# Kernel optimization log

Hardware: AMD Instinct MI355X
Metric: run time of the kernel (lower is better)

## Reference

```python
import jax, jax.numpy as jnp
import numpy as np

ORDER = 3  # truncation level; num_components = ORDER*(ORDER+1)//2 = 6 (independent weights)


def setup_inputs() -> dict:
    key = jax.random.key(0)
    k1, k2, k3 = jax.random.split(key, 3)
    B, T, D, F = 64, 4096, 128, 64
    C = ORDER * (ORDER + 1) // 2
    sequences = jax.random.normal(k1, (B, T, D), dtype=jnp.float32)
    # ls2t_uniform-style init: scaled uniform per component
    kernel = jax.random.normal(k2, (C, D, F), dtype=jnp.float32) / np.sqrt(D)
    bias = jax.random.normal(k3, (C, F), dtype=jnp.float32) * 0.01
    return {"sequences": sequences, "kernel": kernel, "bias": bias}


def _exclusive_cumsum(x, axis):
    # exclusive cumsum = inclusive cumsum minus self (avoids concat/pad allocs)
    return jnp.cumsum(x, axis=axis) - x


def reference(sequences, kernel, bias):
    # sequences: [B, T, D]; kernel: [C, D, F]; bias: [C, F]
    # M[c] = sequences @ kernel[c] + bias[c]  -> [C, B, T, F]
    M = jnp.einsum('btd,cdf->cbtf', sequences, kernel) + bias[:, None, None, :]
    # Level 1: plain sum over time of first component
    Y = [jnp.sum(M[0], axis=1)]  # [B, F]
    k = 1
    for m in range(1, ORDER):
        R = M[k]
        k += 1
        for _ in range(m):
            # iterated-sum recursion: strictly-lower-triangular (exclusive) cumsum over time
            R = M[k] * _exclusive_cumsum(R, axis=1)
            k += 1
        Y.append(jnp.sum(R, axis=1))
    return jnp.stack(Y, axis=-1)  # [B, F, ORDER]
```

## Files before the change

### kernel.cpp

```cpp
#include <hip/hip_runtime.h>
#include <hip/hip_bf16.h>


#define B_ 64
#define T_ 4096
#define D_ 128
#define F_ 64
#define TGROUPS 8
#define TB 512
#define CHT 16
#define NITER (TB / CHT)
#define TPB 512
#define RING 4

typedef __attribute__((ext_vector_type(8))) short short8v;
typedef __attribute__((ext_vector_type(4))) float f32x4;
typedef __attribute__((ext_vector_type(4))) unsigned short ushort4v;

__device__ __forceinline__ unsigned short bfb(float x) {
    __hip_bfloat16 h = __float2bfloat16(x);
    unsigned short u;
    __builtin_memcpy(&u, &h, 2);
    return u;
}

#define BAR() asm volatile("s_waitcnt lgkmcnt(0)\n\ts_barrier" ::: "memory")

__global__ __launch_bounds__(TPB, 2)
void ls2t_kernel(const float* __restrict__ seq,
                 const float* __restrict__ kern,
                 const float* __restrict__ bias,
                 float* __restrict__ ws)
{
    __shared__ unsigned short slds[RING][CHT * D_];

    const int tid  = threadIdx.x;
    const int tg   = blockIdx.x;
    const int b    = blockIdx.y;
    const int lane = tid & 63;
    const int w    = tid >> 6;
    const int cg   = w >> 2;
    const int wv   = w & 3;
    const int fr   = lane & 15;
    const int lg   = lane >> 4;
    const int f    = wv * 16 + fr;

    short8v bfrag[3][4];
    float bc[3];
    #pragma unroll
    for (int cc = 0; cc < 3; ++cc) {
        const int c = cg * 3 + cc;
        bc[cc] = bias[c * F_ + f];
        #pragma unroll
        for (int ks = 0; ks < 4; ++ks) {
            const float* kp = kern + ((size_t)c * D_ + ks * 32 + lg * 8) * F_ + f;
            short8v bf;
            #pragma unroll
            for (int j = 0; j < 8; ++j) bf[j] = (short)bfb(kp[(size_t)j * F_]);
            bfrag[cc][ks] = bf;
        }
    }

    const float* sbase = seq + ((size_t)b * T_ + (size_t)tg * TB) * D_;

    const int srow = tid >> 5;
    const int c4   = tid & 31;
    const int skey = srow & 7;
    const float* g0 = sbase + ((size_t)((srow >> 2) * 128 + (srow & 3))) * D_ + c4 * 4;
    const int woff = srow * D_ + 8 * ((c4 >> 1) ^ skey) + 4 * (c4 & 1);

    #define LD(i) (*reinterpret_cast<const float4*>(g0 + (size_t)(i) * 4 * D_))

    auto wst = [&](int bufi, const float4& v) {
        ushort4v u;
        u[0] = bfb(v.x); u[1] = bfb(v.y); u[2] = bfb(v.z); u[3] = bfb(v.w);
        *reinterpret_cast<ushort4v*>(&slds[bufi][woff]) = u;
    };

    float a0 = 0.f, s1 = 0.f, s2 = 0.f, q2 = 0.f;
    float su = 0.f, sv = 0.f, sw = 0.f, qvu = 0.f, qwv = 0.f, qwvu = 0.f;

    auto compute = [&](int bufi) {
        f32x4 acc[3];
        #pragma unroll
        for (int cc = 0; cc < 3; ++cc)
            acc[cc] = (f32x4){bc[cc], bc[cc], bc[cc], bc[cc]};

        #pragma unroll
        for (int ks = 0; ks < 4; ++ks) {
            const int m0i = ks * 4 + lg;
            short8v a = *reinterpret_cast<const short8v*>(
                &slds[bufi][fr * D_ + 8 * (m0i ^ (fr & 7))]);
            #pragma unroll
            for (int cc = 0; cc < 3; ++cc)
                acc[cc] = __builtin_amdgcn_mfma_f32_16x16x32_bf16(
                    a, bfrag[cc][ks], acc[cc], 0, 0, 0);
        }

        if (cg == 0) {
            #pragma unroll
            for (int r = 0; r < 4; ++r) {
                float m0 = acc[0][r], m1 = acc[1][r], m2 = acc[2][r];
                a0 += m0;
                q2  = fmaf(m2, s1, q2);
                s2 += m2;
                s1 += m1;
            }
        } else {
            #pragma unroll
            for (int r = 0; r < 4; ++r) {
                float m3 = acc[0][r], m4 = acc[1][r], m5 = acc[2][r];
                qwvu = fmaf(m5, qvu, qwvu);
                qwv  = fmaf(m5, sv, qwv);
                sw  += m5;
                qvu  = fmaf(m4, su, qvu);
                sv  += m4;
                su  += m3;
            }
        }
    };

    float4 v0 = LD(0), v1 = LD(1), v2 = LD(2), v3 = LD(3);
    wst(0, v0);
    BAR();

    #pragma unroll 1
    for (int g = 0; g < 7; ++g) {
        const int i = g * 4;
        v0 = LD(i + 4);
        wst(1, v1);
        BAR();
        compute(0);
        v1 = LD(i + 5);
        wst(2, v2);
        BAR();
        compute(1);
        v2 = LD(i + 6);
        wst(3, v3);
        BAR();
        compute(2);
        v3 = LD(i + 7);
        wst(0, v0);
        BAR();
        compute(3);
    }
    wst(1, v1); BAR(); compute(0);
    wst(2, v2); BAR(); compute(1);
    wst(3, v3); BAR(); compute(2);
    compute(3);

    if (cg == 0) {
        #pragma unroll
        for (int m = 16; m <= 32; m <<= 1) {
            float oa0 = __shfl_xor(a0, m), os1 = __shfl_xor(s1, m);
            float os2 = __shfl_xor(s2, m), oq2 = __shfl_xor(q2, m);
            bool up = (lane & m) != 0;
            float Aa0 = up ? oa0 : a0, As1 = up ? os1 : s1;
            float As2 = up ? os2 : s2, Aq2 = up ? oq2 : q2;
            float Ba0 = up ? a0 : oa0, Bs1 = up ? s1 : os1;
            float Bs2 = up ? s2 : os2, Bq2 = up ? q2 : oq2;
            a0 = Aa0 + Ba0;
            q2 = Aq2 + Bq2 + As1 * Bs2;
            s1 = As1 + Bs1;
            s2 = As2 + Bs2;
        }
        if (lg == 0) {
            float* wp = ws + (((size_t)b * TGROUPS + tg) * F_ + f) * 10;
            wp[0] = a0; wp[1] = s1; wp[2] = s2; wp[3] = q2;
        }
    } else {
        #pragma unroll
        for (int m = 16; m <= 32; m <<= 1) {
            float osu = __shfl_xor(su, m),  osv = __shfl_xor(sv, m);
            float osw = __shfl_xor(sw, m),  oqvu = __shfl_xor(qvu, m);
            float oqwv = __shfl_xor(qwv, m), oqwvu = __shfl_xor(qwvu, m);
            bool up = (lane & m) != 0;
            float Asu = up ? osu : su,   Asv = up ? osv : sv;
            float Asw = up ? osw : sw,   Aqvu = up ? oqvu : qvu;
            float Aqwv = up ? oqwv : qwv, Aqwvu = up ? oqwvu : qwvu;
            float Bsu = up ? su : osu,   Bsv = up ? sv : osv;
            float Bsw = up ? sw : osw,   Bqvu = up ? qvu : oqvu;
            float Bqwv = up ? qwv : oqwv, Bqwvu = up ? qwvu : oqwvu;
            qwvu = Aqwvu + Bqwvu + Aqvu * Bsw + Asu * Bqwv;
            qwv  = Aqwv + Bqwv + Asv * Bsw;
            qvu  = Aqvu + Bqvu + Asu * Bsv;
            su = Asu + Bsu;
            sv = Asv + Bsv;
            sw = Asw + Bsw;
        }
        if (lg == 0) {
            float* wp = ws + (((size_t)b * TGROUPS + tg) * F_ + f) * 10;
            wp[4] = su; wp[5] = sv; wp[6] = sw;
            wp[7] = qvu; wp[8] = qwv; wp[9] = qwvu;
        }
    }
    #undef LD
}

struct St { float a0, s1, s2, q2, su, sv, sw, qvu, qwv, qwvu; };

__device__ __forceinline__ St mergeSt(const St& A, const St& B) {
    St r;
    r.a0   = A.a0 + B.a0;
    r.q2   = A.q2 + B.q2 + A.s1 * B.s2;
    r.s1   = A.s1 + B.s1;
    r.s2   = A.s2 + B.s2;
    r.qwvu = A.qwvu + B.qwvu + A.qvu * B.sw + A.su * B.qwv;
    r.qwv  = A.qwv + B.qwv + A.sv * B.sw;
    r.qvu  = A.qvu + B.qvu + A.su * B.sv;
    r.su   = A.su + B.su;
    r.sv   = A.sv + B.sv;
    r.sw   = A.sw + B.sw;
    return r;
}

__global__ __launch_bounds__(64)
void ls2t_fold_kernel(const float* __restrict__ ws, float* __restrict__ out)
{
    const int b = blockIdx.x;
    const int f = threadIdx.x;
    St A = {0, 0, 0, 0, 0, 0, 0, 0, 0, 0};
    #pragma unroll
    for (int g = 0; g < TGROUPS; ++g) {
        const float* rp = ws + (((size_t)b * TGROUPS + g) * F_ + f) * 10;
        St r = {rp[0], rp[1], rp[2], rp[3], rp[4],
                rp[5], rp[6], rp[7], rp[8], rp[9]};
        A = mergeSt(A, r);
    }
    float* op = out + ((size_t)b * F_ + f) * 3;
    op[0] = A.a0;
    op[1] = A.q2;
    op[2] = A.qwvu;
}

extern "C" void kernel_launch(void* const* d_in, const int* in_sizes, int n_in,
                              void* d_out, int out_size, void* d_ws, size_t ws_size,
                              hipStream_t stream) {
    const float* seq  = (const float*)d_in[0];
    const float* kern = (const float*)d_in[1];
    const float* bias = (const float*)d_in[2];
    float* out = (float*)d_out;
    float* ws  = (float*)d_ws;

    dim3 g1(TGROUPS, B_);
    ls2t_kernel<<<g1, TPB, 0, stream>>>(seq, kern, bias, ws);
    ls2t_fold_kernel<<<B_, F_, 0, stream>>>(ws, out);
}
```

Baseline: 45.43 us.

## Double time groups, widen LDS chunks, and use truncating bf16 pack

Halves the time block per workgroup to 256 (16 time groups, 1024 workgroups) and doubles the LDS chunk to 32 rows, with two float4 loads per thread and two 16-row MFMA sub-tiles per chunk. Replaces round-to-nearest bf16 conversion with a byte-permute that truncates the high halves. The aim is more grid parallelism, fewer barriers per row, and cheaper conversion. The cost is a larger LDS ring, more partial states for the fold kernel to merge, and slightly changed rounding.

```diff
diff --git a/kernel.cpp b/kernel.cpp
--- a/kernel.cpp
+++ b/kernel.cpp
@@ -6,16 +6,15 @@
 #define T_ 4096
 #define D_ 128
 #define F_ 64
-#define TGROUPS 8
-#define TB 512
-#define CHT 16
+#define TB 256
+#define TGROUPS (T_ / TB)
+#define CHT 32
 #define NITER (TB / CHT)
 #define TPB 512
 #define RING 4
 
 typedef __attribute__((ext_vector_type(8))) short short8v;
 typedef __attribute__((ext_vector_type(4))) float f32x4;
-typedef __attribute__((ext_vector_type(4))) unsigned short ushort4v;
 
 __device__ __forceinline__ unsigned short bfb(float x) {
     __hip_bfloat16 h = __float2bfloat16(x);
@@ -63,83 +62,110 @@
 
     const float* sbase = seq + ((size_t)b * T_ + (size_t)tg * TB) * D_;
 
-    const int srow = tid >> 5;
-    const int c4   = tid & 31;
-    const int skey = srow & 7;
-    const float* g0 = sbase + ((size_t)((srow >> 2) * 128 + (srow & 3))) * D_ + c4 * 4;
-    const int woff = srow * D_ + 8 * ((c4 >> 1) ^ skey) + 4 * (c4 & 1);
-
-    #define LD(i) (*reinterpret_cast<const float4*>(g0 + (size_t)(i) * 4 * D_))
-
-    auto wst = [&](int bufi, const float4& v) {
-        ushort4v u;
-        u[0] = bfb(v.x); u[1] = bfb(v.y); u[2] = bfb(v.z); u[3] = bfb(v.w);
-        *reinterpret_cast<ushort4v*>(&slds[bufi][woff]) = u;
+    const float* gp[2];
+    int woff[2];
+    #pragma unroll
+    for (int k = 0; k < 2; ++k) {
+        const int u  = k * TPB + tid;
+        const int v  = u >> 5, c4 = u & 31;
+        const int bv = ((v >> 2) & 3) * 64 + ((v >> 4) << 2) + (v & 3);
+        gp[k]   = sbase + (size_t)bv * D_ + c4 * 4;
+        woff[k] = v * D_ + 8 * ((c4 >> 1) ^ (v & 7)) + 4 * (c4 & 1);
+    }
+
+    struct VSet { float4 a, b; };
+    auto issue = [&](int i, VSet& vs) {
+        vs.a = *reinterpret_cast<const float4*>(gp[0] + (size_t)i * 8 * D_);
+        vs.b = *reinterpret_cast<const float4*>(gp[1] + (size_t)i * 8 * D_);
+    };
+    auto wst = [&](int bufi, const VSet& vs) {
+        unsigned short* L = &slds[bufi][0];
+        {
+            unsigned p0 = __builtin_amdgcn_perm(__float_as_uint(vs.a.y),
+                                                __float_as_uint(vs.a.x), 0x07060302u);
+            unsigned p1 = __builtin_amdgcn_perm(__float_as_uint(vs.a.w),
+                                                __float_as_uint(vs.a.z), 0x07060302u);
+            uint2 pv; pv.x = p0; pv.y = p1;
+            *reinterpret_cast<uint2*>(&L[woff[0]]) = pv;
+        }
+        {
+            unsigned p0 = __builtin_amdgcn_perm(__float_as_uint(vs.b.y),
+                                                __float_as_uint(vs.b.x), 0x07060302u);
+            unsigned p1 = __builtin_amdgcn_perm(__float_as_uint(vs.b.w),
+                                                __float_as_uint(vs.b.z), 0x07060302u);
+            uint2 pv; pv.x = p0; pv.y = p1;
+            *reinterpret_cast<uint2*>(&L[woff[1]]) = pv;
+        }
     };
 
     float a0 = 0.f, s1 = 0.f, s2 = 0.f, q2 = 0.f;
     float su = 0.f, sv = 0.f, sw = 0.f, qvu = 0.f, qwv = 0.f, qwvu = 0.f;
 
     auto compute = [&](int bufi) {
-        f32x4 acc[3];
-        #pragma unroll
-        for (int cc = 0; cc < 3; ++cc)
-            acc[cc] = (f32x4){bc[cc], bc[cc], bc[cc], bc[cc]};
-
-        #pragma unroll
-        for (int ks = 0; ks < 4; ++ks) {
-            const int m0i = ks * 4 + lg;
-            short8v a = *reinterpret_cast<const short8v*>(
-                &slds[bufi][fr * D_ + 8 * (m0i ^ (fr & 7))]);
+        #pragma unroll
+        for (int s = 0; s < 2; ++s) {
+            f32x4 acc[3];
             #pragma unroll
             for (int cc = 0; cc < 3; ++cc)
-                acc[cc] = __builtin_amdgcn_mfma_f32_16x16x32_bf16(
-                    a, bfrag[cc][ks], acc[cc], 0, 0, 0);
-        }
-
-        if (cg == 0) {
+                acc[cc] = (f32x4){bc[cc], bc[cc], bc[cc], bc[cc]};
+
             #pragma unroll
-            for (int r = 0; r < 4; ++r) {
-                float m0 = acc[0][r], m1 = acc[1][r], m2 = acc[2][r];
-                a0 += m0;
-                q2  = fmaf(m2, s1, q2);
-                s2 += m2;
-                s1 += m1;
+            for (int ks = 0; ks < 4; ++ks) {
+                short8v a = *reinterpret_cast<const short8v*>(
+                    &slds[bufi][(s * 16 + fr) * D_ + 8 * ((ks * 4 + lg) ^ (fr & 7))]);
+                #pragma unroll
+                for (int cc = 0; cc < 3; ++cc)
+                    acc[cc] = __builtin_amdgcn_mfma_f32_16x16x32_bf16(
+                        a, bfrag[cc][ks], acc[cc], 0, 0, 0);
             }
-        } else {
-            #pragma unroll
-            for (int r = 0; r < 4; ++r) {
-                float m3 = acc[0][r], m4 = acc[1][r], m5 = acc[2][r];
-                qwvu = fmaf(m5, qvu, qwvu);
-                qwv  = fmaf(m5, sv, qwv);
-                sw  += m5;
-                qvu  = fmaf(m4, su, qvu);
-                sv  += m4;
-                su  += m3;
+
+            if (cg == 0) {
+                #pragma unroll
+                for (int r = 0; r < 4; ++r) {
+                    float m0 = acc[0][r], m1 = acc[1][r], m2 = acc[2][r];
+                    a0 += m0;
+                    q2  = fmaf(m2, s1, q2);
+                    s2 += m2;
+                    s1 += m1;
+                }
+            } else {
+                #pragma unroll
+                for (int r = 0; r < 4; ++r) {
+                    float m3 = acc[0][r], m4 = acc[1][r], m5 = acc[2][r];
+                    qwvu = fmaf(m5, qvu, qwvu);
+                    qwv  = fmaf(m5, sv, qwv);
+                    sw  += m5;
+                    qvu  = fmaf(m4, su, qvu);
+                    sv  += m4;
+                    su  += m3;
+                }
             }
         }
     };
 
-    float4 v0 = LD(0), v1 = LD(1), v2 = LD(2), v3 = LD(3);
+    VSet v0, v1, v2, v3;
+    issue(0, v0); issue(1, v1); issue(2, v2); issue(3, v3);
     wst(0, v0);
     BAR();
 
     #pragma unroll 1
-    for (int g = 0; g < 7; ++g) {
-        const int i = g * 4;
-        v0 = LD(i + 4);
+    for (int g = 0; g + 4 < NITER; g += 4) {
+        issue(g + 4, v0);
         wst(1, v1);
         BAR();
         compute(0);
-        v1 = LD(i + 5);
+
+        issue(g + 5, v1);
         wst(2, v2);
         BAR();
         compute(1);
-        v2 = LD(i + 6);
+
+        issue(g + 6, v2);
         wst(3, v3);
         BAR();
         compute(2);
-        v3 = LD(i + 7);
+
+        issue(g + 7, v3);
         wst(0, v0);
         BAR();
         compute(3);
@@ -194,7 +220,6 @@
             wp[7] = qvu; wp[8] = qwv; wp[9] = qwvu;
         }
     }
-    #undef LD
 }
 
 struct St { float a0, s1, s2, q2, su, sv, sw, qvu, qwv, qwvu; };
```

Result: slower. 64.55 us (+42.1%).

## Deepen LDS ring to eight slots and process two chunks per barrier

Applied to the files above, without the earlier changes.

The LDS ring buffer grows from 4 to 8 chunk slots. Each pipeline step now loads, converts and stores two 16-row chunks and runs two MFMA compute passes between barriers, which halves the number of barriers and keeps more global loads in flight. The cost is twice the shared memory per block (32 KB) and more live float4 registers, which could lower occupancy or add register pressure.

```diff
diff --git a/kernel.cpp b/kernel.cpp
--- a/kernel.cpp
+++ b/kernel.cpp
@@ -6,12 +6,12 @@
 #define T_ 4096
 #define D_ 128
 #define F_ 64
-#define TGROUPS 8
 #define TB 512
+#define TGROUPS (T_ / TB)
 #define CHT 16
 #define NITER (TB / CHT)
 #define TPB 512
-#define RING 4
+#define RING 8
 
 typedef __attribute__((ext_vector_type(8))) short short8v;
 typedef __attribute__((ext_vector_type(4))) float f32x4;
@@ -65,9 +65,8 @@
 
     const int srow = tid >> 5;
     const int c4   = tid & 31;
-    const int skey = srow & 7;
     const float* g0 = sbase + ((size_t)((srow >> 2) * 128 + (srow & 3))) * D_ + c4 * 4;
-    const int woff = srow * D_ + 8 * ((c4 >> 1) ^ skey) + 4 * (c4 & 1);
+    const int woff = srow * D_ + 8 * ((c4 >> 1) ^ (srow & 7)) + 4 * (c4 & 1);
 
     #define LD(i) (*reinterpret_cast<const float4*>(g0 + (size_t)(i) * 4 * D_))
 
@@ -120,34 +119,41 @@
         }
     };
 
-    float4 v0 = LD(0), v1 = LD(1), v2 = LD(2), v3 = LD(3);
-    wst(0, v0);
+    float4 w0 = LD(0), w1 = LD(1), w2 = LD(2), w3 = LD(3), w4 = LD(4), w5 = LD(5);
+    float4 w6, w7;
+    wst(0, w0); wst(1, w1);
     BAR();
 
     #pragma unroll 1
-    for (int g = 0; g < 7; ++g) {
-        const int i = g * 4;
-        v0 = LD(i + 4);
-        wst(1, v1);
-        BAR();
-        compute(0);
-        v1 = LD(i + 5);
-        wst(2, v2);
-        BAR();
-        compute(1);
-        v2 = LD(i + 6);
-        wst(3, v3);
-        BAR();
-        compute(2);
-        v3 = LD(i + 7);
-        wst(0, v0);
-        BAR();
-        compute(3);
-    }
-    wst(1, v1); BAR(); compute(0);
-    wst(2, v2); BAR(); compute(1);
-    wst(3, v3); BAR(); compute(2);
-    compute(3);
+    for (int cb = 0; cb < 24; cb += 8) {
+        w6 = LD(cb + 6); w7 = LD(cb + 7);
+        wst(2, w2); wst(3, w3);
+        BAR();
+        compute(0); compute(1);
+        w0 = LD(cb + 8); w1 = LD(cb + 9);
+        wst(4, w4); wst(5, w5);
+        BAR();
+        compute(2); compute(3);
+        w2 = LD(cb + 10); w3 = LD(cb + 11);
+        wst(6, w6); wst(7, w7);
+        BAR();
+        compute(4); compute(5);
+        w4 = LD(cb + 12); w5 = LD(cb + 13);
+        wst(0, w0); wst(1, w1);
+        BAR();
+        compute(6); compute(7);
+    }
+    w6 = LD(30); w7 = LD(31);
+    wst(2, w2); wst(3, w3);
+    BAR();
+    compute(0); compute(1);
+    wst(4, w4); wst(5, w5);
+    BAR();
+    compute(2); compute(3);
+    wst(6, w6); wst(7, w7);
+    BAR();
+    compute(4); compute(5);
+    compute(6); compute(7);
 
     if (cg == 0) {
         #pragma unroll
```

After: 49.12 us. 1.08x slower.
